# Performance work log

Hardware: AMD Instinct MI355X
Metric: run time of the kernel (lower is better)

## Reference

```python
import jax, jax.numpy as jnp
import numpy as np

GAMMA = 1.0

def setup_inputs() -> dict:
    key = jax.random.key(0)
    kx, ky = jax.random.split(key)
    x = jax.random.normal(kx, (8192, 256), dtype=jnp.float32)
    y = jax.random.normal(ky, (8192, 256), dtype=jnp.float32)
    return {"x": x, "y": y}

def reference(x, y):
    # Flatten leading dims as in the original view(-1, d)
    x = x.reshape(-1, x.shape[-1])
    y = y.reshape(-1, y.shape[-1])
    x_sq = jnp.sum(x * x, axis=-1)            # (n_x,)
    y_sq = jnp.sum(y * y, axis=-1)            # (n_y,)
    xy = jnp.einsum('id,jd->ij', x, y)        # (n_x, n_y)
    sq_dist = jnp.maximum(x_sq[:, None] + y_sq[None, :] - 2.0 * xy, 0.0)
    return jnp.exp(-GAMMA * sq_dist)
```

## Files before the change

### kernel.cpp

```cpp
#include <hip/hip_runtime.h>
#include <stdint.h>
#include <stddef.h>

#define NR 8192
#define DD 256
#define BM 128
#define BN 128
#define BKB 128

typedef __attribute__((ext_vector_type(4))) float f32x4;
typedef __attribute__((ext_vector_type(4))) int   i32x4;
typedef __attribute__((ext_vector_type(8))) int   i32x8;

typedef const unsigned int u32c_as1 __attribute__((address_space(1)));
typedef unsigned int u32_as3 __attribute__((address_space(3)));

__global__ __launch_bounds__(256) void rbf_prep(
    const float* __restrict__ x, const float* __restrict__ y,
    uint8_t* __restrict__ xb, uint8_t* __restrict__ yb,
    float* __restrict__ xsq, float* __restrict__ ysq)
{
    int gw = blockIdx.x * 4 + (threadIdx.x >> 6);
    int lane = threadIdx.x & 63;
    const float* src; uint8_t* dst; float* sq; int row;
    if (gw < NR) { src = x; dst = xb; sq = xsq; row = gw; }
    else         { src = y; dst = yb; sq = ysq; row = gw - NR; }

    f32x4 v = *((const f32x4*)(src + (size_t)row * DD) + lane);
    float s = v[0]*v[0] + v[1]*v[1] + v[2]*v[2] + v[3]*v[3];

    int p = __builtin_amdgcn_cvt_pk_fp8_f32(v[0], v[1], 0, false);
    p     = __builtin_amdgcn_cvt_pk_fp8_f32(v[2], v[3], p, true);
    ((int*)dst)[row * 64 + lane] = p;

    #pragma unroll
    for (int m = 32; m; m >>= 1) s += __shfl_xor(s, m, 64);
    if (lane == 0) sq[row] = s;
}

__global__ __launch_bounds__(256, 3) void rbf_mfma(
    const uint8_t* __restrict__ xb, const uint8_t* __restrict__ yb,
    const float* __restrict__ xsq, const float* __restrict__ ysq,
    float* __restrict__ out)
{
    __shared__ __align__(16) uint8_t As[BM * BKB];
    __shared__ __align__(16) uint8_t Bs[BN * BKB];

    const int tid  = threadIdx.x;
    const int wave = tid >> 6;
    const int lane = tid & 63;
    const int r16  = lane & 15;
    const int quad = lane >> 4;
    const int sw   = r16 & 7;

    const int bid    = blockIdx.x;
    const int st     = bid >> 6;
    const int within = bid & 63;
    const int bm_blk = (st >> 3) * 8 + (within >> 3);
    const int bn_blk = (st & 7) * 8 + (within & 7);
    const int bm0    = bm_blk * BM;
    const int bn0    = bn_blk * BN;

    const int wm = (wave >> 1) * 64;
    const int wn = (wave & 1) * 64;

    f32x4 acc[4][4] = {};

    const int chunk_base = wave * 256;

    #pragma unroll
    for (int kt = 0; kt < DD / BKB; ++kt) {
        __syncthreads();
        #pragma unroll
        for (int i = 0; i < 4; ++i) {
            int pos = chunk_base + i * 64 + lane;
            int row = pos >> 3;
            int kc  = (pos & 7) ^ (row & 7);
            const uint8_t* gA = xb + (size_t)(bm0 + row) * DD + kt * BKB + kc * 16;
            __builtin_amdgcn_global_load_lds(
                (u32c_as1*)gA, (u32_as3*)&As[(chunk_base + i * 64) * 16], 16, 0, 0);
        }
        #pragma unroll
        for (int i = 0; i < 4; ++i) {
            int pos = chunk_base + i * 64 + lane;
            int row = pos >> 3;
            int kc  = (pos & 7) ^ (row & 7);
            const uint8_t* gB = yb + (size_t)(bn0 + row) * DD + kt * BKB + kc * 16;
            __builtin_amdgcn_global_load_lds(
                (u32c_as1*)gB, (u32_as3*)&Bs[(chunk_base + i * 64) * 16], 16, 0, 0);
        }
        __syncthreads();

        i32x8 bf[4];
        #pragma unroll
        for (int t = 0; t < 4; ++t) {
            int row = wn + t * 16 + r16;
            i32x4 lo = *(const i32x4*)&Bs[(row * 8 + ((quad * 2    ) ^ sw)) * 16];
            i32x4 hi = *(const i32x4*)&Bs[(row * 8 + ((quad * 2 + 1) ^ sw)) * 16];
            bf[t][0]=lo[0]; bf[t][1]=lo[1]; bf[t][2]=lo[2]; bf[t][3]=lo[3];
            bf[t][4]=hi[0]; bf[t][5]=hi[1]; bf[t][6]=hi[2]; bf[t][7]=hi[3];
        }
        #pragma unroll
        for (int ti = 0; ti < 4; ++ti) {
            int row = wm + ti * 16 + r16;
            i32x4 lo = *(const i32x4*)&As[(row * 8 + ((quad * 2    ) ^ sw)) * 16];
            i32x4 hi = *(const i32x4*)&As[(row * 8 + ((quad * 2 + 1) ^ sw)) * 16];
            i32x8 af;
            af[0]=lo[0]; af[1]=lo[1]; af[2]=lo[2]; af[3]=lo[3];
            af[4]=hi[0]; af[5]=hi[1]; af[6]=hi[2]; af[7]=hi[3];
            #pragma unroll
            for (int tj = 0; tj < 4; ++tj)
                acc[ti][tj] = __builtin_amdgcn_mfma_scale_f32_16x16x128_f8f6f4(
                    af, bf[tj], acc[ti][tj],
                    0, 0,
                    0, 127,
                    0, 127);
        }
    }

    float xs[4][4], ysv[4];
    #pragma unroll
    for (int ti = 0; ti < 4; ++ti)
        #pragma unroll
        for (int r = 0; r < 4; ++r)
            xs[ti][r] = xsq[bm0 + wm + ti * 16 + quad * 4 + r];
    #pragma unroll
    for (int tj = 0; tj < 4; ++tj)
        ysv[tj] = ysq[bn0 + wn + tj * 16 + r16];

    #pragma unroll
    for (int ti = 0; ti < 4; ++ti) {
        #pragma unroll
        for (int tj = 0; tj < 4; ++tj) {
            #pragma unroll
            for (int r = 0; r < 4; ++r) {
                float d = xs[ti][r] + ysv[tj] - 2.0f * acc[ti][tj][r];
                d = fmaxf(d, 0.0f);
                size_t m = (size_t)(bm0 + wm + ti * 16 + quad * 4 + r);
                size_t n = (size_t)(bn0 + wn + tj * 16 + r16);
                out[m * (size_t)NR + n] = __expf(-d);
            }
        }
    }
}

__global__ __launch_bounds__(256) void rbf_fallback(
    const float* __restrict__ x, const float* __restrict__ y, float* __restrict__ out)
{
    __shared__ float xrow[DD];
    int m = blockIdx.x;
    for (int i = threadIdx.x; i < DD; i += 256) xrow[i] = x[(size_t)m * DD + i];
    __syncthreads();
    for (int n = threadIdx.x; n < NR; n += 256) {
        const float* yr = y + (size_t)n * DD;
        float d = 0.f;
        #pragma unroll 8
        for (int k = 0; k < DD; ++k) { float t = xrow[k] - yr[k]; d += t * t; }
        out[(size_t)m * NR + n] = __expf(-fmaxf(d, 0.f));
    }
}

extern "C" void kernel_launch(void* const* d_in, const int* in_sizes, int n_in,
                              void* d_out, int out_size, void* d_ws, size_t ws_size,
                              hipStream_t stream) {
    const float* x = (const float*)d_in[0];
    const float* y = (const float*)d_in[1];
    float* out = (float*)d_out;

    size_t need = (size_t)NR * DD * 2 + (size_t)NR * 4 * 2;
    if (ws_size >= need) {
        uint8_t* xb = (uint8_t*)d_ws;
        uint8_t* yb = xb + (size_t)NR * DD;
        float* xsq = (float*)(yb + (size_t)NR * DD);
        float* ysq = xsq + NR;
        rbf_prep<<<4096, 256, 0, stream>>>(x, y, xb, yb, xsq, ysq);
        rbf_mfma<<<4096, 256, 0, stream>>>(xb, yb, xsq, ysq, out);
    } else {
        rbf_fallback<<<NR, 256, 0, stream>>>(x, y, out);
    }
}
```

Baseline: 290.0 us.

## Stage epilogue through LDS for 128-bit nontemporal output stores

The epilogue previously wrote each MFMA accumulator element as a scalar 4-byte store with a 16-lane row stride, giving poorly coalesced writes to the 256 MB output. Each wave now transposes its accumulator tiles through a padded per-wave LDS buffer that reuses the operand shared memory. Each lane then reads four contiguous dot products and writes a float4 with a nontemporal store. This adds LDS traffic and wait instructions per tile in exchange for wide, coalesced, cache-bypassing global writes.

```diff
diff --git a/kernel.cpp b/kernel.cpp
--- a/kernel.cpp
+++ b/kernel.cpp
@@ -14,6 +14,9 @@
 
 typedef const unsigned int u32c_as1 __attribute__((address_space(1)));
 typedef unsigned int u32_as3 __attribute__((address_space(3)));
+
+#define EPAD 68
+#define EPW  (16 * EPAD)
 
 __global__ __launch_bounds__(256) void rbf_prep(
     const float* __restrict__ x, const float* __restrict__ y,
@@ -43,8 +46,9 @@
     const float* __restrict__ xsq, const float* __restrict__ ysq,
     float* __restrict__ out)
 {
-    __shared__ __align__(16) uint8_t As[BM * BKB];
-    __shared__ __align__(16) uint8_t Bs[BN * BKB];
+    __shared__ __align__(16) uint8_t smem[BM * BKB + BN * BKB];
+    uint8_t* As = smem;
+    uint8_t* Bs = smem + BM * BKB;
 
     const int tid  = threadIdx.x;
     const int wave = tid >> 6;
@@ -118,29 +122,39 @@
         }
     }
 
-    float xs[4][4], ysv[4];
-    #pragma unroll
-    for (int ti = 0; ti < 4; ++ti)
-        #pragma unroll
-        for (int r = 0; r < 4; ++r)
-            xs[ti][r] = xsq[bm0 + wm + ti * 16 + quad * 4 + r];
-    #pragma unroll
-    for (int tj = 0; tj < 4; ++tj)
-        ysv[tj] = ysq[bn0 + wn + tj * 16 + r16];
+    __syncthreads();
+
+    float* wb = (float*)smem + wave * EPW;
+
+    f32x4 ysv = *((const f32x4*)(ysq + bn0 + wn) + r16);
 
     #pragma unroll
     for (int ti = 0; ti < 4; ++ti) {
         #pragma unroll
-        for (int tj = 0; tj < 4; ++tj) {
+        for (int tj = 0; tj < 4; ++tj)
             #pragma unroll
-            for (int r = 0; r < 4; ++r) {
-                float d = xs[ti][r] + ysv[tj] - 2.0f * acc[ti][tj][r];
+            for (int r = 0; r < 4; ++r)
+                wb[(quad * 4 + r) * EPAD + tj * 16 + r16] = acc[ti][tj][r];
+
+        asm volatile("s_waitcnt lgkmcnt(0)" ::: "memory");
+
+        #pragma unroll
+        for (int rep = 0; rep < 4; ++rep) {
+            int lrow = rep * 4 + quad;
+            f32x4 dots = *(const f32x4*)&wb[lrow * EPAD + r16 * 4];
+            int m = bm0 + wm + ti * 16 + lrow;
+            float xs = xsq[m];
+            f32x4 o;
+            #pragma unroll
+            for (int j = 0; j < 4; ++j) {
+                float d = xs + ysv[j] - 2.0f * dots[j];
                 d = fmaxf(d, 0.0f);
-                size_t m = (size_t)(bm0 + wm + ti * 16 + quad * 4 + r);
-                size_t n = (size_t)(bn0 + wn + tj * 16 + r16);
-                out[m * (size_t)NR + n] = __expf(-d);
+                o[j] = __expf(-d);
             }
+            __builtin_nontemporal_store(
+                o, (f32x4*)&out[(size_t)m * NR + bn0 + wn + r16 * 4]);
         }
+        asm volatile("s_waitcnt lgkmcnt(0)" ::: "memory");
     }
 }
 
```

New measurement: 276.5 us. 4.7% less time.
